# Kernel tuning notes

Hardware: AMD Instinct MI355X
Metric: run time of the kernel (lower is better)

The kernel has to match this reference:

```python
import jax, jax.numpy as jnp
import numpy as np

EPS_ATTN = 1e-8  # self.eps is undefined in the torch source; standard slot-attention value
LN_EPS = 1e-5


def _ln(x, g=None, b=None, axes=(-1,)):
    m = x.mean(axes, keepdims=True)
    v = ((x - m) ** 2).mean(axes, keepdims=True)
    y = (x - m) * jax.lax.rsqrt(v + LN_EPS)
    return y * g + b if g is not None else y


def setup_inputs() -> dict:
    key = jax.random.key(0)
    ks = jax.random.split(key, 16)
    B, N, S, d, dh = 16, 4096, 8, 64, 128

    def w(k, shape, fan_in):
        return jax.random.normal(k, shape, jnp.float32) / np.float32(np.sqrt(fan_in))

    return {
        "inputs": jax.random.normal(ks[0], (B, N, d + 2), jnp.float32),
        "slots": jax.random.normal(ks[1], (S, d + 4), jnp.float32),
        "Wq": w(ks[2], (d, d), d),
        "Wk": w(ks[3], (d, d), d),
        "Wv": w(ks[4], (d, d), d),
        "Wg": w(ks[5], (d, 2), 2),
        "bg": jnp.zeros((d,), jnp.float32),
        "ln_pos_g": jnp.ones((d,), jnp.float32),
        "ln_pos_b": jnp.zeros((d,), jnp.float32),
        "W1": w(ks[6], (dh, d), d),
        "b1": jnp.zeros((dh,), jnp.float32),
        "W2": w(ks[7], (d, dh), dh),
        "b2": jnp.zeros((d,), jnp.float32),
        "W_ih": w(ks[8], (3 * d, d), d),
        "W_hh": w(ks[9], (3 * d, d), d),
        "b_ih": jnp.zeros((3 * d,), jnp.float32),
        "b_hh": jnp.zeros((3 * d,), jnp.float32),
        "ln_mlp_g": jnp.ones((d,), jnp.float32),
        "ln_mlp_b": jnp.zeros((d,), jnp.float32),
        "W3": w(ks[10], (dh, d), d),
        "b3": jnp.zeros((dh,), jnp.float32),
        "W4": w(ks[11], (d, dh), dh),
        "b4": jnp.zeros((d,), jnp.float32),
        "ln_slot_g": jnp.ones((d,), jnp.float32),
        "ln_slot_b": jnp.zeros((d,), jnp.float32),
        "n_iters": 3,
    }


def reference(inputs, slots, Wq, Wk, Wv, Wg, bg, ln_pos_g, ln_pos_b, W1, b1, W2, b2,
              W_ih, W_hh, b_ih, b_hh, ln_mlp_g, ln_mlp_b, W3, b3, W4, b4,
              ln_slot_g, ln_slot_b, n_iters):
    feats, grids = inputs[..., :-2], inputs[..., -2:]          # (B,N,d), (B,N,2)
    sl, pos, sc = slots[..., :-4], slots[..., -4:-2], slots[..., -2:]
    B, N, _ = feats.shape
    S, d = sl.shape
    scale = d ** (-0.5)

    slots = jnp.broadcast_to(sl, (B, S, d))
    positions = jnp.clip(jnp.broadcast_to(pos, (B, S, 2)), -1.0, 1.0)
    scales = jnp.clip(jnp.broadcast_to(sc, (B, S, 2)), 1e-3, 2.0)

    k = feats @ Wk.T                                           # (B,N,d)
    v = feats @ Wv.T

    def pos_mlp(x):  # LayerNorm -> Linear -> ReLU -> Linear
        h = _ln(x, ln_pos_g, ln_pos_b)
        h = jax.nn.relu(h @ W1.T + b1)
        return h @ W2.T + b2

    for i_iter in range(n_iters + 1):
        rel = (grids[:, :, None] - positions[:, None]) / scales[:, None]  # (B,N,S,2)
        rgp = rel @ Wg.T + bg                                             # (B,N,S,d)
        k_pos = pos_mlp(k[:, :, None] + rgp)                              # (B,N,S,d)
        v_pos = pos_mlp(v[:, :, None] + rgp)

        slots_n = _ln(slots, ln_slot_g, ln_slot_b)
        q = _ln(slots_n, axes=(-2, -1)) @ Wq.T                            # (B,S,d)

        dots = jnp.einsum('bsd,bnsd->bns', q, k_pos) * scale              # (B,N,S)
        attn = jax.nn.softmax(dots, axis=1) + EPS_ATTN
        attn = attn / attn.sum(axis=-1, keepdims=True)

        updates = jnp.einsum('bns,bnsd->bsd', attn, v_pos)                # (B,S,d)
        positions = jnp.einsum('bns,bnp->bsp', attn, grids)               # (B,S,2)
        spread = (grids[:, :, None] - positions[:, None]) ** 2            # (B,N,S,2)
        scales = jnp.clip(jnp.sqrt(jnp.einsum('bns,bnsp->bsp', attn, spread)), 1e-3, 2.0)

        if i_iter < n_iters:
            x = updates.reshape(-1, d)
            h = slots.reshape(-1, d)
            gi = x @ W_ih.T + b_ih
            gh = h @ W_hh.T + b_hh
            i_r, i_z, i_n = jnp.split(gi, 3, axis=-1)
            h_r, h_z, h_n = jnp.split(gh, 3, axis=-1)
            r = jax.nn.sigmoid(i_r + h_r)
            z = jax.nn.sigmoid(i_z + h_z)
            n_g = jnp.tanh(i_n + r * h_n)
            slots = ((1.0 - z) * n_g + z * h).reshape(B, S, d)
            # slot_mlp (no residual in the source)
            hmlp = jax.nn.relu(_ln(slots, ln_mlp_g, ln_mlp_b) @ W3.T + b3)
            slots = hmlp @ W4.T + b4

    return jnp.concatenate([slots, positions, scales], axis=-1)           # (B,S,d+4)
```

## Files before the change

kernel.cpp:

```cpp
#include <hip/hip_runtime.h>
#include <math.h>

#define BB 16
#define NN 4096
#define SS 8
#define DD 64
#define DHH 128
#define CIN 66
#define NITERS 3
#define LN_EPS_F 1e-5f
#define EPS_ATTN_F 1e-8f
#define QSCALE 0.125f

__device__ __forceinline__ float dot4(float4 a, float4 b) {
    return fmaf(a.x, b.x, fmaf(a.y, b.y, fmaf(a.z, b.z, a.w * b.w)));
}

__global__ __launch_bounds__(256) void k_init_slots(
    const float* __restrict__ slots_in, float* __restrict__ slots,
    float* __restrict__ positions, float* __restrict__ scales) {
    int tid = blockIdx.x * 256 + threadIdx.x;
    if (tid < BB * SS * DD) {
        int s = (tid / DD) % SS;
        int c = tid % DD;
        slots[tid] = slots_in[s * 68 + c];
    }
    if (tid < BB * SS * 2) {
        int s = (tid >> 1) & 7;
        int p = tid & 1;
        float po = slots_in[s * 68 + 64 + p];
        positions[tid] = fminf(fmaxf(po, -1.f), 1.f);
        float sc = slots_in[s * 68 + 66 + p];
        scales[tid] = fminf(fmaxf(sc, 1e-3f), 2.f);
    }
}

__global__ __launch_bounds__(256) void k_prep_w(
    const float* __restrict__ W1, const float* __restrict__ lpg,
    const float* __restrict__ lpb, const float* __restrict__ b1,
    const float* __restrict__ Wg,
    float* __restrict__ W1p, float* __restrict__ avec, float* __restrict__ bvec,
    float* __restrict__ s1vec, float* __restrict__ b1p, float* __restrict__ wgc) {
    __shared__ float w1s[128 * 68];
    int tid = threadIdx.x;
    for (int q = 0; q < 8; q++) {
        int flat = q * 1024 + tid * 4;
        int o = flat >> 6, c = flat & 63;
        *(float4*)(w1s + o * 68 + c) = *(const float4*)(W1 + flat);
    }
    __syncthreads();
    if (tid < 128) {
        int o = tid;
        float a = 0.f, bv = 0.f, s1 = 0.f, b1a = b1[o];
        for (int c = 0; c < 64; c++) {
            float w0 = w1s[o * 68 + c];
            float w = w0 * lpg[c];
            W1p[o * 64 + c] = w;
            a = fmaf(w, Wg[2 * c], a);
            bv = fmaf(w, Wg[2 * c + 1], bv);
            s1 += w;
            b1a = fmaf(w0, lpb[c], b1a);
        }
        avec[o] = a; bvec[o] = bv; s1vec[o] = s1; b1p[o] = b1a;
    }
    if (tid == 128) {
        float mwA = 0.f, mwB = 0.f, AA = 0.f, BBv = 0.f, AB = 0.f;
        for (int c = 0; c < 64; c++) {
            float wa = Wg[2 * c], wb = Wg[2 * c + 1];
            mwA += wa; mwB += wb;
            AA = fmaf(wa, wa, AA); BBv = fmaf(wb, wb, BBv); AB = fmaf(wa, wb, AB);
        }
        wgc[0] = mwA * (1.f / 64.f);
        wgc[1] = mwB * (1.f / 64.f);
        wgc[2] = AA * (1.f / 64.f);
        wgc[3] = BBv * (1.f / 64.f);
        wgc[4] = AB * (2.f / 64.f);
    }
}

__global__ __launch_bounds__(256) void k_prep_w2(
    const float* __restrict__ W1p, const float* __restrict__ Wk,
    const float* __restrict__ Wv, const float* __restrict__ bg,
    float* __restrict__ Wall, float* __restrict__ cu) {
    int flat = blockIdx.x * 256 + threadIdx.x;
    int mat = flat >> 13, rem = flat & 8191;
    int o = rem >> 6, c = rem & 63;
    const float* Wm = mat ? Wv : Wk;
    float acc = 0.f;
    for (int d = 0; d < 64; d++)
        acc = fmaf(W1p[o * 64 + d], Wm[d * 64 + c], acc);
    Wall[flat] = acc;
    if (flat < 128) {
        float a = 0.f;
        for (int d = 0; d < 64; d++) a = fmaf(W1p[flat * 64 + d], bg[d], a);
        cu[flat] = a;
    }
}

__global__ __launch_bounds__(256) void k_prep_main(
    const float* __restrict__ inp, const float* __restrict__ Wall,
    const float* __restrict__ cu, const float* __restrict__ Wk,
    const float* __restrict__ Wv, const float* __restrict__ bg,
    const float* __restrict__ Wg,
    float* __restrict__ uk, float* __restrict__ uv,
    float* __restrict__ kaux, float* __restrict__ vaux, float* __restrict__ gbuf) {
    __shared__ float A[64 * 68];
    __shared__ float Bw[128 * 68];
    __shared__ float wg2[132];
    __shared__ float bgs[64];
    __shared__ float cus[128];
    int tid = threadIdx.x;
    int chunk = blockIdx.y;
    int rowBase = blockIdx.x * 64;
    {
        int r = tid >> 2, cq = (tid & 3) * 16;
        const float* src = inp + (size_t)(rowBase + r) * CIN + cq;
        float* dst = A + r * 68 + cq;
        #pragma unroll
        for (int q = 0; q < 8; q++) {
            float2 tv = *(const float2*)(src + 2 * q);
            dst[2 * q] = tv.x; dst[2 * q + 1] = tv.y;
        }
    }
    if (chunk < 2) {
        const float* Wsrc = Wall + (size_t)chunk * 8192;
        int o = tid >> 1, c0 = (tid & 1) * 32;
        #pragma unroll
        for (int q = 0; q < 8; q++)
            *(float4*)(Bw + o * 68 + c0 + 4 * q) = *(const float4*)(Wsrc + o * 64 + c0 + 4 * q);
        if (tid < 128) cus[tid] = cu[tid];
    } else {
        int o = tid >> 1, c0 = (tid & 1) * 32;
        const float* Wsrc = (o < 64) ? (Wk + o * 64) : (Wv + (o - 64) * 64);
        #pragma unroll
        for (int q = 0; q < 8; q++)
            *(float4*)(Bw + o * 68 + c0 + 4 * q) = *(const float4*)(Wsrc + c0 + 4 * q);
        if (tid < 64) {
            wg2[tid] = Wg[2 * tid]; wg2[66 + tid] = Wg[2 * tid + 1];
            bgs[tid] = bg[tid];
        }
    }
    __syncthreads();
    int r2 = tid >> 3, j = tid & 7;
    float acc0[16], acc1[16];
    #pragma unroll
    for (int q = 0; q < 16; q++) { acc0[q] = 0.f; acc1[q] = 0.f; }
    for (int c4 = 0; c4 < 64; c4 += 4) {
        float4 a0 = *(const float4*)(A + r2 * 68 + c4);
        float4 a1 = *(const float4*)(A + (r2 + 32) * 68 + c4);
        #pragma unroll
        for (int q = 0; q < 16; q++) {
            float4 w = *(const float4*)(Bw + (8 * q + j) * 68 + c4);
            acc0[q] += dot4(a0, w);
            acc1[q] += dot4(a1, w);
        }
    }
    if (chunk < 2) {
        float cub[16];
        #pragma unroll
        for (int q = 0; q < 16; q++) cub[q] = cus[8 * q + j];
        __syncthreads();
        #pragma unroll
        for (int q = 0; q < 16; q++) {
            Bw[r2 * 132 + 8 * q + j] = acc0[q] + cub[q];
            Bw[(r2 + 32) * 132 + 8 * q + j] = acc1[q] + cub[q];
        }
        __syncthreads();
        float* dst = (chunk == 0) ? uk : uv;
        int r = tid >> 2, c0 = (tid & 3) * 32;
        #pragma unroll
        for (int q = 0; q < 8; q++)
            *(float4*)(dst + (size_t)(rowBase + r) * 128 + c0 + 4 * q) =
                *(const float4*)(Bw + r * 132 + c0 + 4 * q);
    } else {
        float mk[2] = {0.f, 0.f}, kk[2] = {0.f, 0.f}, kA[2] = {0.f, 0.f}, kB[2] = {0.f, 0.f};
        float mv[2] = {0.f, 0.f}, vv[2] = {0.f, 0.f}, vA[2] = {0.f, 0.f}, vB[2] = {0.f, 0.f};
        #pragma unroll
        for (int q = 0; q < 8; q++) {
            int ch = 8 * q + j;
            float bgv = bgs[ch], wa = wg2[ch], wb = wg2[66 + ch];
            float x0 = acc0[q] + bgv, x1 = acc1[q] + bgv;
            mk[0] += x0; kk[0] = fmaf(x0, x0, kk[0]); kA[0] = fmaf(x0, wa, kA[0]); kB[0] = fmaf(x0, wb, kB[0]);
            mk[1] += x1; kk[1] = fmaf(x1, x1, kk[1]); kA[1] = fmaf(x1, wa, kA[1]); kB[1] = fmaf(x1, wb, kB[1]);
            float y0 = acc0[q + 8] + bgv, y1 = acc1[q + 8] + bgv;
            mv[0] += y0; vv[0] = fmaf(y0, y0, vv[0]); vA[0] = fmaf(y0, wa, vA[0]); vB[0] = fmaf(y0, wb, vB[0]);
            mv[1] += y1; vv[1] = fmaf(y1, y1, vv[1]); vA[1] = fmaf(y1, wa, vA[1]); vB[1] = fmaf(y1, wb, vB[1]);
        }
        #pragma unroll
        for (int off = 1; off <= 4; off <<= 1) {
            #pragma unroll
            for (int rr = 0; rr < 2; rr++) {
                mk[rr] += __shfl_xor(mk[rr], off, 64); kk[rr] += __shfl_xor(kk[rr], off, 64);
                kA[rr] += __shfl_xor(kA[rr], off, 64); kB[rr] += __shfl_xor(kB[rr], off, 64);
                mv[rr] += __shfl_xor(mv[rr], off, 64); vv[rr] += __shfl_xor(vv[rr], off, 64);
                vA[rr] += __shfl_xor(vA[rr], off, 64); vB[rr] += __shfl_xor(vB[rr], off, 64);
            }
        }
        if (j == 0) {
            #pragma unroll
            for (int rr = 0; rr < 2; rr++) {
                int row = rowBase + r2 + rr * 32;
                float g0 = inp[(size_t)row * CIN + 64];
                float g1 = inp[(size_t)row * CIN + 65];
                float4 m1 = {mk[rr] * (1.f / 64.f), kk[rr] * (1.f / 64.f),
                             kA[rr] * (1.f / 32.f), kB[rr] * (1.f / 32.f)};
                float4 m2 = {g0, g1, 0.f, 0.f};
                *(float4*)(kaux + (size_t)row * 8) = m1;
                *(float4*)(kaux + (size_t)row * 8 + 4) = m2;
                float4 n1 = {mv[rr] * (1.f / 64.f), vv[rr] * (1.f / 64.f),
                             vA[rr] * (1.f / 32.f), vB[rr] * (1.f / 32.f)};
                *(float4*)(vaux + (size_t)row * 8) = n1;
                *(float4*)(vaux + (size_t)row * 8 + 4) = m2;
                *(float2*)(gbuf + (size_t)row * 2) = {g0, g1};
            }
        }
    }
}

__global__ __launch_bounds__(512) void k_slot_prep(
    const float* __restrict__ slots, const float* __restrict__ lsg,
    const float* __restrict__ lsb, const float* __restrict__ Wq,
    const float* __restrict__ W2, const float* __restrict__ b2,
    float* __restrict__ w2q, float* __restrict__ qb2) {
    __shared__ float sn[512];
    __shared__ float qv[SS][64];
    __shared__ float wsum[8], wsum2[8];
    int b = blockIdx.x, t = threadIdx.x;
    int s = t >> 6, c = t & 63;
    float x = slots[(b * SS + s) * DD + c];
    float sum = x;
    for (int off = 32; off; off >>= 1) sum += __shfl_xor(sum, off, 64);
    float m = sum * (1.f / 64.f);
    float dv = x - m;
    float vs = dv * dv;
    for (int off = 32; off; off >>= 1) vs += __shfl_xor(vs, off, 64);
    float y = dv * rsqrtf(vs * (1.f / 64.f) + LN_EPS_F) * lsg[c] + lsb[c];
    float s1 = y, s2 = y * y;
    for (int off = 32; off; off >>= 1) { s1 += __shfl_xor(s1, off, 64); s2 += __shfl_xor(s2, off, 64); }
    if (c == 0) { wsum[s] = s1; wsum2[s] = s2; }
    __syncthreads();
    float ts1 = 0.f, ts2 = 0.f;
    #pragma unroll
    for (int i = 0; i < 8; i++) { ts1 += wsum[i]; ts2 += wsum2[i]; }
    float gm = ts1 * (1.f / 512.f);
    float gv = ts2 * (1.f / 512.f) - gm * gm;
    sn[t] = (y - gm) * rsqrtf(gv + LN_EPS_F);
    __syncthreads();
    float acc = 0.f;
    for (int j4 = 0; j4 < 64; j4 += 4)
        acc += dot4(*(const float4*)&sn[s * 64 + j4], *(const float4*)(Wq + c * 64 + j4));
    qv[s][c] = acc;
    __syncthreads();
    float a0 = 0.f, a1 = 0.f;
    for (int cc = 0; cc < 64; cc++) {
        float qc = qv[s][cc];
        a0 = fmaf(qc, W2[cc * DHH + c], a0);
        a1 = fmaf(qc, W2[cc * DHH + c + 64], a1);
    }
    w2q[(b * SS + s) * DHH + c] = a0 * QSCALE;
    w2q[(b * SS + s) * DHH + c + 64] = a1 * QSCALE;
    float qb = qv[s][c] * b2[c];
    for (int off = 32; off; off >>= 1) qb += __shfl_xor(qb, off, 64);
    if (c == 0) qb2[b * SS + s] = qb * QSCALE;
}

__global__ __launch_bounds__(256) void k_pass1(
    const float* __restrict__ uk, const float* __restrict__ kaux,
    const float* __restrict__ positions, const float* __restrict__ scales,
    const float* __restrict__ avec, const float* __restrict__ bvec,
    const float* __restrict__ s1vec, const float* __restrict__ b1p,
    const float* __restrict__ wgc, const float* __restrict__ w2q,
    const float* __restrict__ qb2, float* __restrict__ dots) {
    int tid = threadIdx.x;
    int chunk = blockIdx.x, b = blockIdx.y;
    int wv = tid >> 6, lane = tid & 63, rh = lane >> 5, ol = lane & 31;
    int o4 = ol * 4;
    float4 a4 = *(const float4*)(avec + o4);
    float4 bv4 = *(const float4*)(bvec + o4);
    float4 s14 = *(const float4*)(s1vec + o4);
    float4 b14 = *(const float4*)(b1p + o4);
    float mwA = wgc[0], mwB = wgc[1], AA = wgc[2], BBc = wgc[3], AB2 = wgc[4];
    float p0[8], p1[8], rc0[8], rc1[8], qb[8];
    float4 wq[8];
    #pragma unroll
    for (int s = 0; s < 8; s++) {
        int bs = b * 8 + s;
        p0[s] = positions[bs * 2]; p1[s] = positions[bs * 2 + 1];
        rc0[s] = 1.f / scales[bs * 2]; rc1[s] = 1.f / scales[bs * 2 + 1];
        qb[s] = qb2[bs];
        wq[s] = *(const float4*)(w2q + (size_t)bs * DHH + o4);
    }
    int row0 = chunk * 64 + wv * 16 + rh;
    size_t rg = (size_t)b * NN + row0;
    float4 m1 = *(const float4*)(kaux + rg * 8);
    float4 m2 = *(const float4*)(kaux + rg * 8 + 4);
    float4 u4 = *(const float4*)(uk + rg * 128 + o4);
    for (int st = 0; st < 8; st++) {
        float4 n1, n2, nu;
        if (st < 7) {
            size_t rgn = rg + (size_t)(st + 1) * 2;
            n1 = *(const float4*)(kaux + rgn * 8);
            n2 = *(const float4*)(kaux + rgn * 8 + 4);
            nu = *(const float4*)(uk + rgn * 128 + o4);
        }
        int row = row0 + st * 2;
        #pragma unroll
        for (int s = 0; s < 8; s++) {
            float rel0 = (m2.x - p0[s]) * rc0[s];
            float rel1 = (m2.y - p1[s]) * rc1[s];
            float m = fmaf(rel1, mwB, fmaf(rel0, mwA, m1.x));
            float q2 = fmaf(rel0, fmaf(rel0, AA, m1.z), m1.y);
            q2 = fmaf(rel1, fmaf(rel1, BBc, m1.w), q2);
            q2 = fmaf(rel0 * rel1, AB2, q2);
            float var = fmaf(-m, m, q2);
            float rstd = rsqrtf(fmaxf(var, 0.f) + LN_EPS_F);
            float p = 0.f, t, h;
            t = fmaf(-m, s14.x, u4.x); t = fmaf(rel0, a4.x, t); t = fmaf(rel1, bv4.x, t);
            h = fmaf(rstd, t, b14.x); p = fmaf(fmaxf(h, 0.f), wq[s].x, p);
            t = fmaf(-m, s14.y, u4.y); t = fmaf(rel0, a4.y, t); t = fmaf(rel1, bv4.y, t);
            h = fmaf(rstd, t, b14.y); p = fmaf(fmaxf(h, 0.f), wq[s].y, p);
            t = fmaf(-m, s14.z, u4.z); t = fmaf(rel0, a4.z, t); t = fmaf(rel1, bv4.z, t);
            h = fmaf(rstd, t, b14.z); p = fmaf(fmaxf(h, 0.f), wq[s].z, p);
            t = fmaf(-m, s14.w, u4.w); t = fmaf(rel0, a4.w, t); t = fmaf(rel1, bv4.w, t);
            h = fmaf(rstd, t, b14.w); p = fmaf(fmaxf(h, 0.f), wq[s].w, p);
            p += __shfl_xor(p, 1, 64);
            p += __shfl_xor(p, 2, 64);
            p += __shfl_xor(p, 4, 64);
            p += __shfl_xor(p, 8, 64);
            p += __shfl_xor(p, 16, 64);
            if (ol == 0)
                dots[(size_t)(b * 8 + s) * NN + row] = p + qb[s];
        }
        m1 = n1; m2 = n2; u4 = nu;
    }
}

__global__ __launch_bounds__(256) void k_pass2(
    const float* __restrict__ uv, const float* __restrict__ vaux,
    const float* __restrict__ positions, const float* __restrict__ scales,
    const float* __restrict__ avec, const float* __restrict__ bvec,
    const float* __restrict__ s1vec, const float* __restrict__ b1p,
    const float* __restrict__ wgc, const float* __restrict__ attn,
    float* __restrict__ H) {
    __shared__ float Hw[4 * 1024];
    int tid = threadIdx.x;
    int chunk = blockIdx.x, b = blockIdx.y;
    int wv = tid >> 6, lane = tid & 63, rh = lane >> 5, ol = lane & 31;
    int o4 = ol * 4;
    float4 a4 = *(const float4*)(avec + o4);
    float4 bv4 = *(const float4*)(bvec + o4);
    float4 s14 = *(const float4*)(s1vec + o4);
    float4 b14 = *(const float4*)(b1p + o4);
    float mwA = wgc[0], mwB = wgc[1], AA = wgc[2], BBc = wgc[3], AB2 = wgc[4];
    float p0[8], p1[8], rc0[8], rc1[8];
    #pragma unroll
    for (int s = 0; s < 8; s++) {
        int bs = b * 8 + s;
        p0[s] = positions[bs * 2]; p1[s] = positions[bs * 2 + 1];
        rc0[s] = 1.f / scales[bs * 2]; rc1[s] = 1.f / scales[bs * 2 + 1];
    }
    float hq[8][4];
    #pragma unroll
    for (int s = 0; s < 8; s++)
        #pragma unroll
        for (int c = 0; c < 4; c++) hq[s][c] = 0.f;
    int row0 = chunk * 64 + wv * 16 + rh;
    size_t rg = (size_t)b * NN + row0;
    float4 m1 = *(const float4*)(vaux + rg * 8);
    float4 m2 = *(const float4*)(vaux + rg * 8 + 4);
    float4 u4 = *(const float4*)(uv + rg * 128 + o4);
    for (int st = 0; st < 8; st++) {
        float4 n1, n2, nu;
        if (st < 7) {
            size_t rgn = rg + (size_t)(st + 1) * 2;
            n1 = *(const float4*)(vaux + rgn * 8);
            n2 = *(const float4*)(vaux + rgn * 8 + 4);
            nu = *(const float4*)(uv + rgn * 128 + o4);
        }
        int row = row0 + st * 2;
        #pragma unroll
        for (int s = 0; s < 8; s++) {
            float ar = attn[(size_t)(b * 8 + s) * NN + row];
            float rel0 = (m2.x - p0[s]) * rc0[s];
            float rel1 = (m2.y - p1[s]) * rc1[s];
            float m = fmaf(rel1, mwB, fmaf(rel0, mwA, m1.x));
            float q2 = fmaf(rel0, fmaf(rel0, AA, m1.z), m1.y);
            q2 = fmaf(rel1, fmaf(rel1, BBc, m1.w), q2);
            q2 = fmaf(rel0 * rel1, AB2, q2);
            float var = fmaf(-m, m, q2);
            float rstd = rsqrtf(fmaxf(var, 0.f) + LN_EPS_F);
            float t, h;
            t = fmaf(-m, s14.x, u4.x); t = fmaf(rel0, a4.x, t); t = fmaf(rel1, bv4.x, t);
            h = fmaf(rstd, t, b14.x); hq[s][0] = fmaf(ar, fmaxf(h, 0.f), hq[s][0]);
            t = fmaf(-m, s14.y, u4.y); t = fmaf(rel0, a4.y, t); t = fmaf(rel1, bv4.y, t);
            h = fmaf(rstd, t, b14.y); hq[s][1] = fmaf(ar, fmaxf(h, 0.f), hq[s][1]);
            t = fmaf(-m, s14.z, u4.z); t = fmaf(rel0, a4.z, t); t = fmaf(rel1, bv4.z, t);
            h = fmaf(rstd, t, b14.z); hq[s][2] = fmaf(ar, fmaxf(h, 0.f), hq[s][2]);
            t = fmaf(-m, s14.w, u4.w); t = fmaf(rel0, a4.w, t); t = fmaf(rel1, bv4.w, t);
            h = fmaf(rstd, t, b14.w); hq[s][3] = fmaf(ar, fmaxf(h, 0.f), hq[s][3]);
        }
        m1 = n1; m2 = n2; u4 = nu;
    }
    #pragma unroll
    for (int s = 0; s < 8; s++)
        #pragma unroll
        for (int c = 0; c < 4; c++)
            hq[s][c] += __shfl_xor(hq[s][c], 32, 64);
    if (lane < 32) {
        #pragma unroll
        for (int s = 0; s < 8; s++) {
            float4 st = {hq[s][0], hq[s][1], hq[s][2], hq[s][3]};
            *(float4*)(Hw + wv * 1024 + s * 128 + o4) = st;
        }
    }
    __syncthreads();
    #pragma unroll
    for (int q = 0; q < 4; q++) {
        int flat = q * 256 + tid;
        float sum = Hw[flat] + Hw[1024 + flat] + Hw[2048 + flat] + Hw[3072 + flat];
        atomicAdd(&H[(size_t)b * 8 * DHH + flat], sum);
    }
}

__global__ __launch_bounds__(256) void k_softmax_ms(
    const float* __restrict__ dots, float* __restrict__ Mv, float* __restrict__ Lv,
    float* __restrict__ H) {
    __shared__ float red[4];
    int bs = blockIdx.x, t = threadIdx.x;
    if (t < 128) H[(size_t)bs * DHH + t] = 0.f;
    const float* dp = dots + (size_t)bs * NN;
    float mx = -1e30f;
    #pragma unroll
    for (int it = 0; it < 4; it++) {
        float4 d = *(const float4*)(dp + it * 1024 + t * 4);
        mx = fmaxf(mx, fmaxf(fmaxf(d.x, d.y), fmaxf(d.z, d.w)));
    }
    for (int off = 32; off; off >>= 1) mx = fmaxf(mx, __shfl_xor(mx, off, 64));
    if ((t & 63) == 0) red[t >> 6] = mx;
    __syncthreads();
    float M = fmaxf(fmaxf(red[0], red[1]), fmaxf(red[2], red[3]));
    __syncthreads();
    float sm = 0.f;
    #pragma unroll
    for (int it = 0; it < 4; it++) {
        float4 d = *(const float4*)(dp + it * 1024 + t * 4);
        sm += expf(d.x - M) + expf(d.y - M) + expf(d.z - M) + expf(d.w - M);
    }
    for (int off = 32; off; off >>= 1) sm += __shfl_xor(sm, off, 64);
    if ((t & 63) == 0) red[t >> 6] = sm;
    __syncthreads();
    if (t == 0) { Mv[bs] = M; Lv[bs] = red[0] + red[1] + red[2] + red[3]; }
}

__global__ __launch_bounds__(256) void k_attn(
    const float* __restrict__ dots, const float* __restrict__ Mv,
    const float* __restrict__ Lv, float* __restrict__ attn) {
    int chunk = blockIdx.x, b = blockIdx.y;
    int n = chunk * 256 + threadIdx.x;
    float a[8];
    float rs = 0.f;
    #pragma unroll
    for (int s = 0; s < 8; s++) {
        int bs = b * 8 + s;
        float d = dots[(size_t)bs * NN + n];
        a[s] = expf(d - Mv[bs]) * (1.f / Lv[bs]) + EPS_ATTN_F;
        rs += a[s];
    }
    float inv = 1.f / rs;
    #pragma unroll
    for (int s = 0; s < 8; s++)
        attn[(size_t)(b * 8 + s) * NN + n] = a[s] * inv;
}

__global__ __launch_bounds__(256) void k_stats(
    const float* __restrict__ attn, const float* __restrict__ gbuf,
    float* __restrict__ positions, float* __restrict__ scales,
    float* __restrict__ stats) {
    __shared__ float red[4][5];
    int bs = blockIdx.x, b = bs >> 3, t = threadIdx.x;
    const float* ap = attn + (size_t)bs * NN;
    const float* gb = gbuf + (size_t)b * NN * 2;
    float v0 = 0.f, v1 = 0.f, v2 = 0.f, v3 = 0.f, v4 = 0.f;
    #pragma unroll
    for (int it = 0; it < 4; it++) {
        int n0 = it * 1024 + t * 4;
        float4 av = *(const float4*)(ap + n0);
        float4 g1 = *(const float4*)(gb + (size_t)n0 * 2);
        float4 g2 = *(const float4*)(gb + (size_t)n0 * 2 + 4);
        v0 += av.x + av.y + av.z + av.w;
        v1 = fmaf(av.x, g1.x, fmaf(av.y, g1.z, fmaf(av.z, g2.x, fmaf(av.w, g2.z, v1))));
        v2 = fmaf(av.x, g1.y, fmaf(av.y, g1.w, fmaf(av.z, g2.y, fmaf(av.w, g2.w, v2))));
        v3 = fmaf(av.x, g1.x * g1.x, fmaf(av.y, g1.z * g1.z, fmaf(av.z, g2.x * g2.x, fmaf(av.w, g2.z * g2.z, v3))));
        v4 = fmaf(av.x, g1.y * g1.y, fmaf(av.y, g1.w * g1.w, fmaf(av.z, g2.y * g2.y, fmaf(av.w, g2.w * g2.w, v4))));
    }
    for (int off = 32; off; off >>= 1) {
        v0 += __shfl_xor(v0, off, 64); v1 += __shfl_xor(v1, off, 64);
        v2 += __shfl_xor(v2, off, 64); v3 += __shfl_xor(v3, off, 64);
        v4 += __shfl_xor(v4, off, 64);
    }
    if ((t & 63) == 0) {
        int w = t >> 6;
        red[w][0] = v0; red[w][1] = v1; red[w][2] = v2; red[w][3] = v3; red[w][4] = v4;
    }
    __syncthreads();
    if (t == 0) {
        float A0 = red[0][0] + red[1][0] + red[2][0] + red[3][0];
        float A1x = red[0][1] + red[1][1] + red[2][1] + red[3][1];
        float A1y = red[0][2] + red[1][2] + red[2][2] + red[3][2];
        float A2x = red[0][3] + red[1][3] + red[2][3] + red[3][3];
        float A2y = red[0][4] + red[1][4] + red[2][4] + red[3][4];
        positions[bs * 2 + 0] = A1x;
        positions[bs * 2 + 1] = A1y;
        float sx = A2x - A1x * A1x * (2.f - A0);
        float sy = A2y - A1y * A1y * (2.f - A0);
        scales[bs * 2 + 0] = fminf(fmaxf(sqrtf(fmaxf(sx, 0.f)), 1e-3f), 2.f);
        scales[bs * 2 + 1] = fminf(fmaxf(sqrtf(fmaxf(sy, 0.f)), 1e-3f), 2.f);
        stats[bs] = A0;
    }
}

__global__ __launch_bounds__(64) void k_gru_mlp(
    const float* __restrict__ H, const float* __restrict__ stats,
    const float* __restrict__ W2, const float* __restrict__ b2,
    const float* __restrict__ W_ih, const float* __restrict__ W_hh,
    const float* __restrict__ b_ih, const float* __restrict__ b_hh,
    const float* __restrict__ lmg, const float* __restrict__ lmb,
    const float* __restrict__ W3, const float* __restrict__ b3,
    const float* __restrict__ W4, const float* __restrict__ b4,
    float* __restrict__ slots) {
    int bs = blockIdx.x;
    int c = threadIdx.x;
    __shared__ float hl[DHH], ul[DD], sl[DD], yl[DD], hml[DHH];
    hl[c] = H[bs * DHH + c];
    hl[c + 64] = H[bs * DHH + 64 + c];
    float hold = slots[bs * DD + c];
    sl[c] = hold;
    __syncthreads();
    float A0 = stats[bs];
    float u = A0 * b2[c];
    for (int o = 0; o < DHH; o += 4) {
        float4 w = *(const float4*)(W2 + c * DHH + o);
        u = fmaf(w.x, hl[o], fmaf(w.y, hl[o + 1], fmaf(w.z, hl[o + 2], fmaf(w.w, hl[o + 3], u))));
    }
    ul[c] = u;
    __syncthreads();
    float gir = b_ih[c], giz = b_ih[64 + c], gin = b_ih[128 + c];
    float ghr = b_hh[c], ghz = b_hh[64 + c], ghn = b_hh[128 + c];
    for (int k4 = 0; k4 < DD; k4 += 4) {
        float4 uu = *(const float4*)(ul + k4);
        float4 hh = *(const float4*)(sl + k4);
        gir += dot4(uu, *(const float4*)(W_ih + c * DD + k4));
        giz += dot4(uu, *(const float4*)(W_ih + (64 + c) * DD + k4));
        gin += dot4(uu, *(const float4*)(W_ih + (128 + c) * DD + k4));
        ghr += dot4(hh, *(const float4*)(W_hh + c * DD + k4));
        ghz += dot4(hh, *(const float4*)(W_hh + (64 + c) * DD + k4));
        ghn += dot4(hh, *(const float4*)(W_hh + (128 + c) * DD + k4));
    }
    float rg = 1.f / (1.f + expf(-(gir + ghr)));
    float zg = 1.f / (1.f + expf(-(giz + ghz)));
    float ng = tanhf(gin + rg * ghn);
    float snew = (1.f - zg) * ng + zg * hold;
    float sum = snew;
    for (int off = 32; off; off >>= 1) sum += __shfl_xor(sum, off, 64);
    float m = sum * (1.f / 64.f);
    float dv = snew - m;
    float vv = dv * dv;
    for (int off = 32; off; off >>= 1) vv += __shfl_xor(vv, off, 64);
    yl[c] = dv * rsqrtf(vv * (1.f / 64.f) + LN_EPS_F) * lmg[c] + lmb[c];
    __syncthreads();
    float h0 = b3[c], h1 = b3[64 + c];
    for (int k4 = 0; k4 < DD; k4 += 4) {
        float4 yy = *(const float4*)(yl + k4);
        h0 += dot4(yy, *(const float4*)(W3 + c * DD + k4));
        h1 += dot4(yy, *(const float4*)(W3 + (64 + c) * DD + k4));
    }
    hml[c] = fmaxf(h0, 0.f);
    hml[64 + c] = fmaxf(h1, 0.f);
    __syncthreads();
    float outv = b4[c];
    for (int o4 = 0; o4 < DHH; o4 += 4) {
        float4 hm4 = *(const float4*)(hml + o4);
        outv += dot4(hm4, *(const float4*)(W4 + c * DHH + o4));
    }
    slots[bs * DD + c] = outv;
}

__global__ __launch_bounds__(256) void k_write_out(
    const float* __restrict__ slots, const float* __restrict__ positions,
    const float* __restrict__ scales, float* __restrict__ out) {
    int tid = blockIdx.x * 256 + threadIdx.x;
    if (tid >= BB * SS * 68) return;
    int bs = tid / 68, c = tid % 68;
    float v;
    if (c < 64) v = slots[bs * 64 + c];
    else if (c < 66) v = positions[bs * 2 + (c - 64)];
    else v = scales[bs * 2 + (c - 66)];
    out[tid] = v;
}

extern "C" void kernel_launch(void* const* d_in, const int* in_sizes, int n_in,
                              void* d_out, int out_size, void* d_ws, size_t ws_size,
                              hipStream_t stream) {
    (void)in_sizes; (void)n_in; (void)out_size; (void)ws_size;
    const float* inp = (const float*)d_in[0];
    const float* slots_in = (const float*)d_in[1];
    const float* Wq = (const float*)d_in[2];
    const float* Wk = (const float*)d_in[3];
    const float* Wv = (const float*)d_in[4];
    const float* Wg = (const float*)d_in[5];
    const float* bg = (const float*)d_in[6];
    const float* lpg = (const float*)d_in[7];
    const float* lpb = (const float*)d_in[8];
    const float* W1 = (const float*)d_in[9];
    const float* b1 = (const float*)d_in[10];
    const float* W2 = (const float*)d_in[11];
    const float* b2 = (const float*)d_in[12];
    const float* W_ih = (const float*)d_in[13];
    const float* W_hh = (const float*)d_in[14];
    const float* b_ih = (const float*)d_in[15];
    const float* b_hh = (const float*)d_in[16];
    const float* lmg = (const float*)d_in[17];
    const float* lmb = (const float*)d_in[18];
    const float* W3 = (const float*)d_in[19];
    const float* b3 = (const float*)d_in[20];
    const float* W4 = (const float*)d_in[21];
    const float* b4 = (const float*)d_in[22];
    const float* lsg = (const float*)d_in[23];
    const float* lsb = (const float*)d_in[24];
    float* out = (float*)d_out;
    float* ws = (float*)d_ws;

    const size_t NR = (size_t)BB * NN;
    size_t o_uk = 0;
    size_t o_uv = o_uk + NR * 128;
    size_t o_kaux = o_uv + NR * 128;
    size_t o_vaux = o_kaux + NR * 8;
    size_t o_gbuf = o_vaux + NR * 8;
    size_t o_dots = o_gbuf + NR * 2;
    size_t o_attn = o_dots + NR * SS;
    size_t o_slots = o_attn + NR * SS;
    size_t o_pos = o_slots + BB * SS * DD;
    size_t o_scl = o_pos + BB * SS * 2;
    size_t o_w2q = o_scl + BB * SS * 2;
    size_t o_qb2 = o_w2q + BB * SS * DHH;
    size_t o_Mv = o_qb2 + BB * SS;
    size_t o_Lv = o_Mv + BB * SS;
    size_t o_H = o_Lv + BB * SS;
    size_t o_stats = o_H + BB * SS * DHH;
    size_t o_W1p = o_stats + BB * SS;
    size_t o_avec = o_W1p + DHH * DD;
    size_t o_bvec = o_avec + DHH;
    size_t o_s1v = o_bvec + DHH;
    size_t o_b1p = o_s1v + DHH;
    size_t o_wgc = o_b1p + DHH;
    size_t o_Wall = o_wgc + 8;
    size_t o_cu = o_Wall + 2 * DHH * DD;

    float* uk = ws + o_uk;
    float* uv = ws + o_uv;
    float* kaux = ws + o_kaux;
    float* vaux = ws + o_vaux;
    float* gbuf = ws + o_gbuf;
    float* dots = ws + o_dots;
    float* attn = ws + o_attn;
    float* slots = ws + o_slots;
    float* positions = ws + o_pos;
    float* scales = ws + o_scl;
    float* w2q = ws + o_w2q;
    float* qb2 = ws + o_qb2;
    float* Mv = ws + o_Mv;
    float* Lv = ws + o_Lv;
    float* H = ws + o_H;
    float* stats = ws + o_stats;
    float* W1p = ws + o_W1p;
    float* avec = ws + o_avec;
    float* bvec = ws + o_bvec;
    float* s1v = ws + o_s1v;
    float* b1p = ws + o_b1p;
    float* wgc = ws + o_wgc;
    float* Wall = ws + o_Wall;
    float* cu = ws + o_cu;

    k_init_slots<<<32, 256, 0, stream>>>(slots_in, slots, positions, scales);
    k_prep_w<<<1, 256, 0, stream>>>(W1, lpg, lpb, b1, Wg, W1p, avec, bvec, s1v, b1p, wgc);
    k_prep_w2<<<64, 256, 0, stream>>>(W1p, Wk, Wv, bg, Wall, cu);
    k_prep_main<<<dim3(1024, 3), 256, 0, stream>>>(inp, Wall, cu, Wk, Wv, bg, Wg,
                                                   uk, uv, kaux, vaux, gbuf);

    for (int it = 0; it <= NITERS; ++it) {
        k_slot_prep<<<BB, 512, 0, stream>>>(slots, lsg, lsb, Wq, W2, b2, w2q, qb2);
        k_pass1<<<dim3(64, BB), 256, 0, stream>>>(uk, kaux, positions, scales,
                                                  avec, bvec, s1v, b1p, wgc, w2q, qb2, dots);
        k_softmax_ms<<<BB * SS, 256, 0, stream>>>(dots, Mv, Lv, H);
        k_attn<<<dim3(16, BB), 256, 0, stream>>>(dots, Mv, Lv, attn);
        if (it < NITERS) {
            k_pass2<<<dim3(64, BB), 256, 0, stream>>>(uv, vaux, positions, scales,
                                                      avec, bvec, s1v, b1p, wgc, attn, H);
            k_stats<<<BB * SS, 256, 0, stream>>>(attn, gbuf, positions, scales, stats);
            k_gru_mlp<<<BB * SS, 64, 0, stream>>>(H, stats, W2, b2, W_ih, W_hh, b_ih, b_hh,
                                                  lmg, lmb, W3, b3, W4, b4, slots);
        } else {
            k_stats<<<BB * SS, 256, 0, stream>>>(attn, gbuf, positions, scales, stats);
        }
    }
    k_write_out<<<34, 256, 0, stream>>>(slots, positions, scales, out);
}
```

Before: 474.9 us.

## Fuse attention stats into attn kernel and merge GRU/MLP with slot prep

The position/scale statistics are now accumulated inside the attention-normalisation kernel using wave shuffles, shared atomics and global atomics, which removes the separate k_stats pass and the gbuf buffer. The GRU/MLP kernel now processes all 8 slots of a batch per block and performs the next iteration's slot-prep (LayerNorm, Wq and W2 projections) itself, so k_slot_prep only runs once before the loop. This cuts kernel launches and one re-read of attn per iteration. The cost is float atomics, which make the accumulation order nondeterministic, and fewer, larger blocks for the GRU stage (16 instead of 128).

```diff
diff --git a/kernel.cpp b/kernel.cpp
--- a/kernel.cpp
+++ b/kernel.cpp
@@ -103,7 +103,7 @@
     const float* __restrict__ Wv, const float* __restrict__ bg,
     const float* __restrict__ Wg,
     float* __restrict__ uk, float* __restrict__ uv,
-    float* __restrict__ kaux, float* __restrict__ vaux, float* __restrict__ gbuf) {
+    float* __restrict__ kaux, float* __restrict__ vaux) {
     __shared__ float A[64 * 68];
     __shared__ float Bw[128 * 68];
     __shared__ float wg2[132];
@@ -211,7 +211,6 @@
                              vA[rr] * (1.f / 32.f), vB[rr] * (1.f / 32.f)};
                 *(float4*)(vaux + (size_t)row * 8) = n1;
                 *(float4*)(vaux + (size_t)row * 8 + 4) = m2;
-                *(float2*)(gbuf + (size_t)row * 2) = {g0, g1};
             }
         }
     }
@@ -424,10 +423,11 @@
 
 __global__ __launch_bounds__(256) void k_softmax_ms(
     const float* __restrict__ dots, float* __restrict__ Mv, float* __restrict__ Lv,
-    float* __restrict__ H) {
+    float* __restrict__ H, float* __restrict__ stats5) {
     __shared__ float red[4];
     int bs = blockIdx.x, t = threadIdx.x;
     if (t < 128) H[(size_t)bs * DHH + t] = 0.f;
+    if (t < 5) stats5[bs * 5 + t] = 0.f;
     const float* dp = dots + (size_t)bs * NN;
     float mx = -1e30f;
     #pragma unroll
@@ -452,103 +452,107 @@
     if (t == 0) { Mv[bs] = M; Lv[bs] = red[0] + red[1] + red[2] + red[3]; }
 }
 
-__global__ __launch_bounds__(256) void k_attn(
+__global__ __launch_bounds__(256) void k_attn_stats(
     const float* __restrict__ dots, const float* __restrict__ Mv,
-    const float* __restrict__ Lv, float* __restrict__ attn) {
+    const float* __restrict__ Lv, const float* __restrict__ kaux,
+    float* __restrict__ attn, float* __restrict__ stats5) {
+    __shared__ float stS[40];
+    __shared__ float Ml[8], Rl[8];
     int chunk = blockIdx.x, b = blockIdx.y;
-    int n = chunk * 256 + threadIdx.x;
+    int t = threadIdx.x;
+    if (t < 8) { Ml[t] = Mv[b * 8 + t]; Rl[t] = 1.f / Lv[b * 8 + t]; }
+    if (t >= 8 && t < 48) stS[t - 8] = 0.f;
+    __syncthreads();
+    int n = chunk * 256 + t;
     float a[8];
     float rs = 0.f;
     #pragma unroll
     for (int s = 0; s < 8; s++) {
-        int bs = b * 8 + s;
-        float d = dots[(size_t)bs * NN + n];
-        a[s] = expf(d - Mv[bs]) * (1.f / Lv[bs]) + EPS_ATTN_F;
+        float d = dots[(size_t)(b * 8 + s) * NN + n];
+        a[s] = expf(d - Ml[s]) * Rl[s] + EPS_ATTN_F;
         rs += a[s];
     }
     float inv = 1.f / rs;
     #pragma unroll
-    for (int s = 0; s < 8; s++)
-        attn[(size_t)(b * 8 + s) * NN + n] = a[s] * inv;
-}
-
-__global__ __launch_bounds__(256) void k_stats(
-    const float* __restrict__ attn, const float* __restrict__ gbuf,
+    for (int s = 0; s < 8; s++) {
+        a[s] *= inv;
+        attn[(size_t)(b * 8 + s) * NN + n] = a[s];
+    }
+    float2 g = *(const float2*)(kaux + ((size_t)b * NN + n) * 8 + 4);
+    int lane = t & 63;
+    #pragma unroll
+    for (int s = 0; s < 8; s++) {
+        float v0 = a[s];
+        float v1 = a[s] * g.x, v2 = a[s] * g.y;
+        float v3 = v1 * g.x, v4 = v2 * g.y;
+        for (int off = 32; off; off >>= 1) {
+            v0 += __shfl_xor(v0, off, 64); v1 += __shfl_xor(v1, off, 64);
+            v2 += __shfl_xor(v2, off, 64); v3 += __shfl_xor(v3, off, 64);
+            v4 += __shfl_xor(v4, off, 64);
+        }
+        if (lane == 0) {
+            atomicAdd(&stS[s * 5 + 0], v0);
+            atomicAdd(&stS[s * 5 + 1], v1);
+            atomicAdd(&stS[s * 5 + 2], v2);
+            atomicAdd(&stS[s * 5 + 3], v3);
+            atomicAdd(&stS[s * 5 + 4], v4);
+        }
+    }
+    __syncthreads();
+    if (t < 40) atomicAdd(&stats5[b * 40 + t], stS[t]);
+}
+
+__global__ __launch_bounds__(512) void k_gru_fused(
+    const float* __restrict__ H, const float* __restrict__ stats5,
     float* __restrict__ positions, float* __restrict__ scales,
-    float* __restrict__ stats) {
-    __shared__ float red[4][5];
-    int bs = blockIdx.x, b = bs >> 3, t = threadIdx.x;
-    const float* ap = attn + (size_t)bs * NN;
-    const float* gb = gbuf + (size_t)b * NN * 2;
-    float v0 = 0.f, v1 = 0.f, v2 = 0.f, v3 = 0.f, v4 = 0.f;
-    #pragma unroll
-    for (int it = 0; it < 4; it++) {
-        int n0 = it * 1024 + t * 4;
-        float4 av = *(const float4*)(ap + n0);
-        float4 g1 = *(const float4*)(gb + (size_t)n0 * 2);
-        float4 g2 = *(const float4*)(gb + (size_t)n0 * 2 + 4);
-        v0 += av.x + av.y + av.z + av.w;
-        v1 = fmaf(av.x, g1.x, fmaf(av.y, g1.z, fmaf(av.z, g2.x, fmaf(av.w, g2.z, v1))));
-        v2 = fmaf(av.x, g1.y, fmaf(av.y, g1.w, fmaf(av.z, g2.y, fmaf(av.w, g2.w, v2))));
-        v3 = fmaf(av.x, g1.x * g1.x, fmaf(av.y, g1.z * g1.z, fmaf(av.z, g2.x * g2.x, fmaf(av.w, g2.z * g2.z, v3))));
-        v4 = fmaf(av.x, g1.y * g1.y, fmaf(av.y, g1.w * g1.w, fmaf(av.z, g2.y * g2.y, fmaf(av.w, g2.w * g2.w, v4))));
-    }
-    for (int off = 32; off; off >>= 1) {
-        v0 += __shfl_xor(v0, off, 64); v1 += __shfl_xor(v1, off, 64);
-        v2 += __shfl_xor(v2, off, 64); v3 += __shfl_xor(v3, off, 64);
-        v4 += __shfl_xor(v4, off, 64);
-    }
-    if ((t & 63) == 0) {
-        int w = t >> 6;
-        red[w][0] = v0; red[w][1] = v1; red[w][2] = v2; red[w][3] = v3; red[w][4] = v4;
-    }
-    __syncthreads();
-    if (t == 0) {
-        float A0 = red[0][0] + red[1][0] + red[2][0] + red[3][0];
-        float A1x = red[0][1] + red[1][1] + red[2][1] + red[3][1];
-        float A1y = red[0][2] + red[1][2] + red[2][2] + red[3][2];
-        float A2x = red[0][3] + red[1][3] + red[2][3] + red[3][3];
-        float A2y = red[0][4] + red[1][4] + red[2][4] + red[3][4];
-        positions[bs * 2 + 0] = A1x;
-        positions[bs * 2 + 1] = A1y;
-        float sx = A2x - A1x * A1x * (2.f - A0);
-        float sy = A2y - A1y * A1y * (2.f - A0);
-        scales[bs * 2 + 0] = fminf(fmaxf(sqrtf(fmaxf(sx, 0.f)), 1e-3f), 2.f);
-        scales[bs * 2 + 1] = fminf(fmaxf(sqrtf(fmaxf(sy, 0.f)), 1e-3f), 2.f);
-        stats[bs] = A0;
-    }
-}
-
-__global__ __launch_bounds__(64) void k_gru_mlp(
-    const float* __restrict__ H, const float* __restrict__ stats,
     const float* __restrict__ W2, const float* __restrict__ b2,
     const float* __restrict__ W_ih, const float* __restrict__ W_hh,
     const float* __restrict__ b_ih, const float* __restrict__ b_hh,
     const float* __restrict__ lmg, const float* __restrict__ lmb,
     const float* __restrict__ W3, const float* __restrict__ b3,
     const float* __restrict__ W4, const float* __restrict__ b4,
-    float* __restrict__ slots) {
-    int bs = blockIdx.x;
-    int c = threadIdx.x;
-    __shared__ float hl[DHH], ul[DD], sl[DD], yl[DD], hml[DHH];
-    hl[c] = H[bs * DHH + c];
-    hl[c + 64] = H[bs * DHH + 64 + c];
+    const float* __restrict__ lsg, const float* __restrict__ lsb,
+    const float* __restrict__ Wq,
+    float* __restrict__ slots, float* __restrict__ w2q, float* __restrict__ qb2) {
+    __shared__ float hl[SS][DHH], ul[SS][DD], sl[SS][DD], yl[SS][DD], hml[SS][DHH];
+    __shared__ float a0s[8];
+    __shared__ float sn[512];
+    __shared__ float qv[SS][64];
+    __shared__ float wsum[8], wsum2[8];
+    int b = blockIdx.x, t = threadIdx.x;
+    int s = t >> 6, c = t & 63;
+    int bs = b * SS + s;
+    if (t < 8) {
+        int bss = b * SS + t;
+        float A0 = stats5[bss * 5 + 0];
+        float A1x = stats5[bss * 5 + 1], A1y = stats5[bss * 5 + 2];
+        float A2x = stats5[bss * 5 + 3], A2y = stats5[bss * 5 + 4];
+        positions[bss * 2 + 0] = A1x;
+        positions[bss * 2 + 1] = A1y;
+        float sx = A2x - A1x * A1x * (2.f - A0);
+        float sy = A2y - A1y * A1y * (2.f - A0);
+        scales[bss * 2 + 0] = fminf(fmaxf(sqrtf(fmaxf(sx, 0.f)), 1e-3f), 2.f);
+        scales[bss * 2 + 1] = fminf(fmaxf(sqrtf(fmaxf(sy, 0.f)), 1e-3f), 2.f);
+        a0s[t] = A0;
+    }
+    hl[s][c] = H[(size_t)bs * DHH + c];
+    hl[s][c + 64] = H[(size_t)bs * DHH + 64 + c];
     float hold = slots[bs * DD + c];
-    sl[c] = hold;
-    __syncthreads();
-    float A0 = stats[bs];
+    sl[s][c] = hold;
+    __syncthreads();
+    float A0 = a0s[s];
     float u = A0 * b2[c];
     for (int o = 0; o < DHH; o += 4) {
         float4 w = *(const float4*)(W2 + c * DHH + o);
-        u = fmaf(w.x, hl[o], fmaf(w.y, hl[o + 1], fmaf(w.z, hl[o + 2], fmaf(w.w, hl[o + 3], u))));
-    }
-    ul[c] = u;
+        u = fmaf(w.x, hl[s][o], fmaf(w.y, hl[s][o + 1], fmaf(w.z, hl[s][o + 2], fmaf(w.w, hl[s][o + 3], u))));
+    }
+    ul[s][c] = u;
     __syncthreads();
     float gir = b_ih[c], giz = b_ih[64 + c], gin = b_ih[128 + c];
     float ghr = b_hh[c], ghz = b_hh[64 + c], ghn = b_hh[128 + c];
     for (int k4 = 0; k4 < DD; k4 += 4) {
-        float4 uu = *(const float4*)(ul + k4);
-        float4 hh = *(const float4*)(sl + k4);
+        float4 uu = *(const float4*)(&ul[s][k4]);
+        float4 hh = *(const float4*)(&sl[s][k4]);
         gir += dot4(uu, *(const float4*)(W_ih + c * DD + k4));
         giz += dot4(uu, *(const float4*)(W_ih + (64 + c) * DD + k4));
         gin += dot4(uu, *(const float4*)(W_ih + (128 + c) * DD + k4));
@@ -566,35 +570,81 @@
     float dv = snew - m;
     float vv = dv * dv;
     for (int off = 32; off; off >>= 1) vv += __shfl_xor(vv, off, 64);
-    yl[c] = dv * rsqrtf(vv * (1.f / 64.f) + LN_EPS_F) * lmg[c] + lmb[c];
+    yl[s][c] = dv * rsqrtf(vv * (1.f / 64.f) + LN_EPS_F) * lmg[c] + lmb[c];
     __syncthreads();
     float h0 = b3[c], h1 = b3[64 + c];
     for (int k4 = 0; k4 < DD; k4 += 4) {
-        float4 yy = *(const float4*)(yl + k4);
+        float4 yy = *(const float4*)(&yl[s][k4]);
         h0 += dot4(yy, *(const float4*)(W3 + c * DD + k4));
         h1 += dot4(yy, *(const float4*)(W3 + (64 + c) * DD + k4));
     }
-    hml[c] = fmaxf(h0, 0.f);
-    hml[64 + c] = fmaxf(h1, 0.f);
+    hml[s][c] = fmaxf(h0, 0.f);
+    hml[s][64 + c] = fmaxf(h1, 0.f);
     __syncthreads();
     float outv = b4[c];
     for (int o4 = 0; o4 < DHH; o4 += 4) {
-        float4 hm4 = *(const float4*)(hml + o4);
+        float4 hm4 = *(const float4*)(&hml[s][o4]);
         outv += dot4(hm4, *(const float4*)(W4 + c * DHH + o4));
     }
     slots[bs * DD + c] = outv;
+    float x = outv;
+    float sums = x;
+    for (int off = 32; off; off >>= 1) sums += __shfl_xor(sums, off, 64);
+    float ms = sums * (1.f / 64.f);
+    float dvs = x - ms;
+    float vss = dvs * dvs;
+    for (int off = 32; off; off >>= 1) vss += __shfl_xor(vss, off, 64);
+    float y = dvs * rsqrtf(vss * (1.f / 64.f) + LN_EPS_F) * lsg[c] + lsb[c];
+    float s1 = y, s2 = y * y;
+    for (int off = 32; off; off >>= 1) { s1 += __shfl_xor(s1, off, 64); s2 += __shfl_xor(s2, off, 64); }
+    if (c == 0) { wsum[s] = s1; wsum2[s] = s2; }
+    __syncthreads();
+    float ts1 = 0.f, ts2 = 0.f;
+    #pragma unroll
+    for (int i = 0; i < 8; i++) { ts1 += wsum[i]; ts2 += wsum2[i]; }
+    float gm = ts1 * (1.f / 512.f);
+    float gv = ts2 * (1.f / 512.f) - gm * gm;
+    sn[t] = (y - gm) * rsqrtf(gv + LN_EPS_F);
+    __syncthreads();
+    float acc = 0.f;
+    for (int j4 = 0; j4 < 64; j4 += 4)
+        acc += dot4(*(const float4*)&sn[s * 64 + j4], *(const float4*)(Wq + c * 64 + j4));
+    qv[s][c] = acc;
+    __syncthreads();
+    float a0 = 0.f, a1 = 0.f;
+    for (int cc = 0; cc < 64; cc++) {
+        float qc = qv[s][cc];
+        a0 = fmaf(qc, W2[cc * DHH + c], a0);
+        a1 = fmaf(qc, W2[cc * DHH + c + 64], a1);
+    }
+    w2q[(size_t)bs * DHH + c] = a0 * QSCALE;
+    w2q[(size_t)bs * DHH + c + 64] = a1 * QSCALE;
+    float qb = qv[s][c] * b2[c];
+    for (int off = 32; off; off >>= 1) qb += __shfl_xor(qb, off, 64);
+    if (c == 0) qb2[bs] = qb * QSCALE;
 }
 
 __global__ __launch_bounds__(256) void k_write_out(
-    const float* __restrict__ slots, const float* __restrict__ positions,
-    const float* __restrict__ scales, float* __restrict__ out) {
+    const float* __restrict__ slots, const float* __restrict__ stats5,
+    float* __restrict__ out) {
     int tid = blockIdx.x * 256 + threadIdx.x;
     if (tid >= BB * SS * 68) return;
     int bs = tid / 68, c = tid % 68;
     float v;
-    if (c < 64) v = slots[bs * 64 + c];
-    else if (c < 66) v = positions[bs * 2 + (c - 64)];
-    else v = scales[bs * 2 + (c - 66)];
+    if (c < 64) {
+        v = slots[bs * 64 + c];
+    } else {
+        float A0 = stats5[bs * 5 + 0];
+        if (c < 66) {
+            v = stats5[bs * 5 + 1 + (c - 64)];
+        } else {
+            int p = c - 66;
+            float A1 = stats5[bs * 5 + 1 + p];
+            float A2 = stats5[bs * 5 + 3 + p];
+            float sx = A2 - A1 * A1 * (2.f - A0);
+            v = fminf(fmaxf(sqrtf(fmaxf(sx, 0.f)), 1e-3f), 2.f);
+        }
+    }
     out[tid] = v;
 }
 
@@ -635,8 +685,7 @@
     size_t o_uv = o_uk + NR * 128;
     size_t o_kaux = o_uv + NR * 128;
     size_t o_vaux = o_kaux + NR * 8;
-    size_t o_gbuf = o_vaux + NR * 8;
-    size_t o_dots = o_gbuf + NR * 2;
+    size_t o_dots = o_vaux + NR * 8;
     size_t o_attn = o_dots + NR * SS;
     size_t o_slots = o_attn + NR * SS;
     size_t o_pos = o_slots + BB * SS * DD;
@@ -646,8 +695,8 @@
     size_t o_Mv = o_qb2 + BB * SS;
     size_t o_Lv = o_Mv + BB * SS;
     size_t o_H = o_Lv + BB * SS;
-    size_t o_stats = o_H + BB * SS * DHH;
-    size_t o_W1p = o_stats + BB * SS;
+    size_t o_st5 = o_H + BB * SS * DHH;
+    size_t o_W1p = o_st5 + BB * SS * 5;
     size_t o_avec = o_W1p + DHH * DD;
     size_t o_bvec = o_avec + DHH;
     size_t o_s1v = o_bvec + DHH;
@@ -660,7 +709,6 @@
     float* uv = ws + o_uv;
     float* kaux = ws + o_kaux;
     float* vaux = ws + o_vaux;
-    float* gbuf = ws + o_gbuf;
     float* dots = ws + o_dots;
     float* attn = ws + o_attn;
     float* slots = ws + o_slots;
@@ -671,7 +719,7 @@
     float* Mv = ws + o_Mv;
     float* Lv = ws + o_Lv;
     float* H = ws + o_H;
-    float* stats = ws + o_stats;
+    float* stats5 = ws + o_st5;
     float* W1p = ws + o_W1p;
     float* avec = ws + o_avec;
     float* bvec = ws + o_bvec;
@@ -685,23 +733,22 @@
     k_prep_w<<<1, 256, 0, stream>>>(W1, lpg, lpb, b1, Wg, W1p, avec, bvec, s1v, b1p, wgc);
     k_prep_w2<<<64, 256, 0, stream>>>(W1p, Wk, Wv, bg, Wall, cu);
     k_prep_main<<<dim3(1024, 3), 256, 0, stream>>>(inp, Wall, cu, Wk, Wv, bg, Wg,
-                                                   uk, uv, kaux, vaux, gbuf);
+                                                   uk, uv, kaux, vaux);
+    k_slot_prep<<<BB, 512, 0, stream>>>(slots, lsg, lsb, Wq, W2, b2, w2q, qb2);
 
     for (int it = 0; it <= NITERS; ++it) {
-        k_slot_prep<<<BB, 512, 0, stream>>>(slots, lsg, lsb, Wq, W2, b2, w2q, qb2);
         k_pass1<<<dim3(64, BB), 256, 0, stream>>>(uk, kaux, positions, scales,
                                                   avec, bvec, s1v, b1p, wgc, w2q, qb2, dots);
-        k_softmax_ms<<<BB * SS, 256, 0, stream>>>(dots, Mv, Lv, H);
-        k_attn<<<dim3(16, BB), 256, 0, stream>>>(dots, Mv, Lv, attn);
+        k_softmax_ms<<<BB * SS, 256, 0, stream>>>(dots, Mv, Lv, H, stats5);
+        k_attn_stats<<<dim3(16, BB), 256, 0, stream>>>(dots, Mv, Lv, kaux, attn, stats5);
         if (it < NITERS) {
             k_pass2<<<dim3(64, BB), 256, 0, stream>>>(uv, vaux, positions, scales,
                                                       avec, bvec, s1v, b1p, wgc, attn, H);
-            k_stats<<<BB * SS, 256, 0, stream>>>(attn, gbuf, positions, scales, stats);
-            k_gru_mlp<<<BB * SS, 64, 0, stream>>>(H, stats, W2, b2, W_ih, W_hh, b_ih, b_hh,
-                                                  lmg, lmb, W3, b3, W4, b4, slots);
-        } else {
-            k_stats<<<BB * SS, 256, 0, stream>>>(attn, gbuf, positions, scales, stats);
-        }
-    }
-    k_write_out<<<34, 256, 0, stream>>>(slots, positions, scales, out);
-}
+            k_gru_fused<<<BB, 512, 0, stream>>>(H, stats5, positions, scales,
+                                                W2, b2, W_ih, W_hh, b_ih, b_hh,
+                                                lmg, lmb, W3, b3, W4, b4,
+                                                lsg, lsb, Wq, slots, w2q, qb2);
+        }
+    }
+    k_write_out<<<34, 256, 0, stream>>>(slots, stats5, out);
+}
```

Result: slower. 590.4 us (+24.3%).
